# Optimization experiments

Measured on AMD Instinct MI355X. Metric: run time of the kernel, lower is better.

The kernel has to match this reference:

```python
import jax, jax.numpy as jnp
import numpy as np

ALPHA = 16.0
R = 8.0
SCALE = ALPHA / R  # scaling = alpha / r, same for every adapter


def setup_inputs() -> dict:
    key = jax.random.key(0)
    ks = jax.random.split(key, 5)
    B_, S, D = 4, 2048, 4096
    E, r = 8, 8
    x = jax.random.normal(ks[0], (B_, S, D), dtype=jnp.float32)
    W = jax.random.normal(ks[1], (D, D), dtype=jnp.float32) * (1.0 / np.sqrt(D))
    b = jax.random.normal(ks[2], (D,), dtype=jnp.float32) * 0.02
    A = jax.random.normal(ks[3], (E, r, D), dtype=jnp.float32) * (1.0 / np.sqrt(D))
    Bm = jax.random.normal(ks[4], (E, D, r), dtype=jnp.float32) * 0.02
    return {"x": x, "W": W, "b": b, "A": A, "B": Bm}


def reference(x, W, b, A, B):
    # base = F.linear(x, W, b)
    base = jnp.einsum('bsi,oi->bso', x, W) + b
    # lora_total = sum_e scale * (x @ A_e.T @ B_e.T); all experts stacked.
    # intermediate [B,S,E,r] is tiny (r=8)
    t = jnp.einsum('bsi,eri->bser', x, A)
    lora = jnp.einsum('bser,eor->bso', t, B) * SCALE
    return base + lora
```

## Files before the change

kernel.cpp:

```cpp
#include <hip/hip_runtime.h>
#include <hip/hip_bf16.h>

typedef unsigned short u16;
typedef __bf16 bf16x8 __attribute__((ext_vector_type(8)));
typedef float f32x4 __attribute__((ext_vector_type(4)));

constexpr int Mdim = 8192;
constexpr int Ndim = 4096;
constexpr int Kdim = 4096;
constexpr int ER   = 64;
constexpr float LSCALE = 2.0f;

__device__ __forceinline__ u16 f2bf(float f) {
    union { float f; unsigned u; } v; v.f = f;
    unsigned r = v.u + 0x7fffu + ((v.u >> 16) & 1u);
    return (u16)(r >> 16);
}

#define GLOAD_LDS16(g, l)                                             \
    __builtin_amdgcn_global_load_lds(                                 \
        (const __attribute__((address_space(1))) void*)(g),           \
        (__attribute__((address_space(3))) void*)(l), 16, 0, 0)

__global__ __launch_bounds__(256) void weff_kernel(
    const float* __restrict__ W, const float* __restrict__ A,
    const float* __restrict__ Bm, u16* __restrict__ Wb)
{
    __shared__ __align__(16) float sAc[ER][128];
    __shared__ __align__(16) float sBc[64][ER];

    const int t  = threadIdx.x;
    const int i0 = blockIdx.x * 128;
    const int o0 = blockIdx.y * 64;

#pragma unroll
    for (int p = 0; p < 8; ++p) {
        int lin = p * 1024 + t * 4;
        int er = lin >> 7, ci = lin & 127;
        *(float4*)&sAc[er][ci] = *(const float4*)(A + (size_t)er * Kdim + i0 + ci);
    }
    {
        int ol = t >> 2;
        int c  = (t & 3) * 16;
#pragma unroll
        for (int q = 0; q < 2; ++q) {
            int er = c + q * 8;
            int e  = er >> 3;
            const float* src = Bm + ((size_t)e * Ndim + (o0 + ol)) * 8;
            *(float4*)&sBc[ol][er]     = *(const float4*)(src);
            *(float4*)&sBc[ol][er + 4] = *(const float4*)(src + 4);
        }
    }
    __syncthreads();

    const int tx = t & 31;
    const int ty = t >> 5;
    float acc[8][4] = {};
#pragma unroll 4
    for (int er = 0; er < ER; ++er) {
        float4 a = *(const float4*)&sAc[er][tx * 4];
#pragma unroll
        for (int q = 0; q < 8; ++q) {
            float bv = sBc[q * 8 + ty][er];
            acc[q][0] += bv * a.x;
            acc[q][1] += bv * a.y;
            acc[q][2] += bv * a.z;
            acc[q][3] += bv * a.w;
        }
    }
#pragma unroll
    for (int q = 0; q < 8; ++q) {
        int o = o0 + q * 8 + ty;
        const float4 w = *(const float4*)(W + (size_t)o * Kdim + i0 + tx * 4);
        ushort4 st;
        st.x = f2bf(w.x + LSCALE * acc[q][0]);
        st.y = f2bf(w.y + LSCALE * acc[q][1]);
        st.z = f2bf(w.z + LSCALE * acc[q][2]);
        st.w = f2bf(w.w + LSCALE * acc[q][3]);
        *(ushort4*)(Wb + (size_t)o * Kdim + i0 + tx * 4) = st;
    }
}

__global__ __launch_bounds__(256) void cvt_x_kernel(
    const float* __restrict__ x, u16* __restrict__ xb)
{
    size_t i = (size_t)blockIdx.x * blockDim.x + threadIdx.x;
    const float4 v0 = *(const float4*)(x + i * 8);
    const float4 v1 = *(const float4*)(x + i * 8 + 4);
    uint4 o;
    o.x = (unsigned)f2bf(v0.x) | ((unsigned)f2bf(v0.y) << 16);
    o.y = (unsigned)f2bf(v0.z) | ((unsigned)f2bf(v0.w) << 16);
    o.z = (unsigned)f2bf(v1.x) | ((unsigned)f2bf(v1.y) << 16);
    o.w = (unsigned)f2bf(v1.z) | ((unsigned)f2bf(v1.w) << 16);
    *(uint4*)(xb + i * 8) = o;
}

constexpr int BM = 256, BN = 256, BK = 64;
constexpr int NT = Kdim / BK;

__global__ __launch_bounds__(512, 2) void gemm_bias_kernel(
    const u16* __restrict__ Xb, const u16* __restrict__ Wb,
    const float* __restrict__ bias, float* __restrict__ C)
{
    __shared__ __align__(16) u16 lds[65536];

    const int t    = threadIdx.x;
    const int lane = t & 63;
    const int wv   = t >> 6;
    const int wr   = wv >> 2;
    const int wc   = wv & 3;

    const int wg  = blockIdx.x;
    const int xcd = wg & 7, lid = wg >> 3;
    const int mt  = (xcd & 1) * 16 + (lid >> 2);
    const int ntl = (xcd >> 1) * 4 + (lid & 3);
    const int bm  = mt * BM;
    const int bn  = ntl * BN;

    u16* sA0 = lds;          u16* sA1 = lds + 16384;
    u16* sB0 = lds + 32768;  u16* sB1 = lds + 49152;

    const u16* aSrc[4]; const u16* bSrc[4]; int dOff[4];
#pragma unroll
    for (int i = 0; i < 4; ++i) {
        int c   = i * 512 + t;
        int cs  = c ^ (((c >> 5) & 1) << 1) ^ (((c >> 6) & 1) << 2);
        int row = c >> 3;
        int col = (cs & 7) * 8;
        aSrc[i] = Xb + (size_t)(bm + row) * Kdim + col;
        bSrc[i] = Wb + (size_t)(bn + row) * Kdim + col;
        dOff[i] = i * 4096 + t * 8;
    }

    const int rl  = (lane & 15) * 64;
    const int sx  = (((lane >> 2) & 1) << 4) | (((lane >> 3) & 1) << 5);
    const int cp0 = (((lane >> 4) * 8)) ^ sx;
    const int cp1 = (32 + (lane >> 4) * 8) ^ sx;
    const int aBase = wr * 8192 + rl;
    const int bBase = wc * 4096 + rl;

    f32x4 acc[8][4];
#pragma unroll
    for (int i = 0; i < 8; ++i)
#pragma unroll
        for (int j = 0; j < 4; ++j)
            acc[i][j] = f32x4{0.f, 0.f, 0.f, 0.f};

    bf16x8 af[4][2];
    bf16x8 bfr[4][2];

#define LOADA(SRC, MH)                                                        \
    _Pragma("unroll")                                                         \
    for (int mi = 0; mi < 4; ++mi) {                                          \
        af[mi][0] = *(const bf16x8*)&SRC[aBase + ((MH)*4 + mi) * 1024 + cp0]; \
        af[mi][1] = *(const bf16x8*)&SRC[aBase + ((MH)*4 + mi) * 1024 + cp1]; \
    }

#define LOADB(SRC, NH)                                                        \
    _Pragma("unroll")                                                         \
    for (int nl = 0; nl < 2; ++nl) {                                          \
        bfr[(NH)*2 + nl][0] = *(const bf16x8*)&SRC[bBase + ((NH)*2 + nl) * 1024 + cp0]; \
        bfr[(NH)*2 + nl][1] = *(const bf16x8*)&SRC[bBase + ((NH)*2 + nl) * 1024 + cp1]; \
    }

#define MQ(MH, NH)                                                            \
    __builtin_amdgcn_s_setprio(1);                                            \
    _Pragma("unroll")                                                         \
    for (int mi = 0; mi < 4; ++mi)                                            \
        _Pragma("unroll")                                                     \
        for (int nl = 0; nl < 2; ++nl) {                                      \
            acc[(MH)*4 + mi][(NH)*2 + nl] =                                   \
                __builtin_amdgcn_mfma_f32_16x16x32_bf16(                      \
                    af[mi][0], bfr[(NH)*2 + nl][0],                           \
                    acc[(MH)*4 + mi][(NH)*2 + nl], 0, 0, 0);                  \
            acc[(MH)*4 + mi][(NH)*2 + nl] =                                   \
                __builtin_amdgcn_mfma_f32_16x16x32_bf16(                      \
                    af[mi][1], bfr[(NH)*2 + nl][1],                           \
                    acc[(MH)*4 + mi][(NH)*2 + nl], 0, 0, 0);                  \
        }                                                                     \
    __builtin_amdgcn_s_setprio(0);

#define ITER(CURA, CURB, NXA, NXB, DOISS, VMS)                                \
    {                                                                         \
        if (DOISS) {                                                          \
            _Pragma("unroll")                                                 \
            for (int i = 0; i < 4; ++i)                                       \
                GLOAD_LDS16(aSrc[i] + koff, (NXA) + dOff[i]);                 \
            _Pragma("unroll")                                                 \
            for (int i = 0; i < 4; ++i)                                       \
                GLOAD_LDS16(bSrc[i] + koff, (NXB) + dOff[i]);                 \
            koff += 64;                                                       \
        }                                                                     \
        asm volatile("s_waitcnt vmcnt(" VMS ")" ::: "memory");                \
        __builtin_amdgcn_s_barrier();                                         \
        asm volatile("" ::: "memory");                                        \
        LOADA(CURA, 0); LOADB(CURB, 0); MQ(0, 0);                             \
        LOADB(CURB, 1); MQ(0, 1);                                             \
        LOADA(CURA, 1); MQ(1, 1);                                             \
        MQ(1, 0);                                                             \
        asm volatile("s_waitcnt lgkmcnt(0)" ::: "memory");                    \
        __builtin_amdgcn_s_barrier();                                         \
        asm volatile("" ::: "memory");                                        \
    }

#pragma unroll
    for (int i = 0; i < 4; ++i) GLOAD_LDS16(aSrc[i], sA0 + dOff[i]);
#pragma unroll
    for (int i = 0; i < 4; ++i) GLOAD_LDS16(bSrc[i], sB0 + dOff[i]);

    int koff = 64;

#pragma unroll 1
    for (int t2 = 0; t2 < NT - 2; t2 += 2) {
        ITER(sA0, sB0, sA1, sB1, 1, "8");
        ITER(sA1, sB1, sA0, sB0, 1, "8");
    }
    ITER(sA0, sB0, sA1, sB1, 1, "8");
    ITER(sA1, sB1, sA0, sB0, 0, "0");

#undef ITER
#undef MQ
#undef LOADB
#undef LOADA

#pragma unroll
    for (int ni = 0; ni < 4; ++ni) {
        const int col = bn + wc * 64 + ni * 16 + (lane & 15);
        const float bv = bias[col];
#pragma unroll
        for (int mi = 0; mi < 8; ++mi) {
            const int rbase = bm + wr * 128 + mi * 16 + (lane >> 4) * 4;
#pragma unroll
            for (int j = 0; j < 4; ++j)
                C[(size_t)(rbase + j) * Ndim + col] = acc[mi][ni][j] + bv;
        }
    }
}

__global__ __launch_bounds__(256) void naive_row_kernel(
    const float* __restrict__ x, const float* __restrict__ W,
    const float* __restrict__ bias, const float* __restrict__ A,
    const float* __restrict__ Bm, float* __restrict__ out)
{
    __shared__ float sx[Kdim];
    __shared__ float st[ER];
    const int m = blockIdx.x;
    const float* xr = x + (size_t)m * Kdim;
    for (int i = threadIdx.x; i < Kdim; i += 256) sx[i] = xr[i];
    __syncthreads();
    if (threadIdx.x < ER) {
        const float* ar = A + (size_t)threadIdx.x * Kdim;
        float s = 0.f;
        for (int i = 0; i < Kdim; ++i) s += sx[i] * ar[i];
        st[threadIdx.x] = s;
    }
    __syncthreads();
    for (int o = threadIdx.x; o < Ndim; o += 256) {
        const float* wr = W + (size_t)o * Kdim;
        float s = bias[o];
        for (int i = 0; i < Kdim; ++i) s += sx[i] * wr[i];
        float l = 0.f;
        for (int e = 0; e < 8; ++e) {
            const float* bp = Bm + ((size_t)e * Ndim + o) * 8;
            for (int r = 0; r < 8; ++r) l += st[e * 8 + r] * bp[r];
        }
        out[(size_t)m * Ndim + o] = s + LSCALE * l;
    }
}

extern "C" void kernel_launch(void* const* d_in, const int* in_sizes, int n_in,
                              void* d_out, int out_size, void* d_ws, size_t ws_size,
                              hipStream_t stream)
{
    const float* x  = (const float*)d_in[0];
    const float* W  = (const float*)d_in[1];
    const float* b  = (const float*)d_in[2];
    const float* A  = (const float*)d_in[3];
    const float* Bm = (const float*)d_in[4];
    float* out = (float*)d_out;

    const size_t xb_bytes = (size_t)Mdim * Kdim * 2;
    const size_t wb_bytes = (size_t)Ndim * Kdim * 2;

    if (ws_size >= xb_bytes + wb_bytes) {
        u16* Xb = (u16*)d_ws;
        u16* Wb = (u16*)((char*)d_ws + xb_bytes);
        cvt_x_kernel<<<(Mdim * (size_t)Kdim) / 8 / 256, 256, 0, stream>>>(x, Xb);
        weff_kernel<<<dim3(Kdim / 128, Ndim / 64), 256, 0, stream>>>(W, A, Bm, Wb);
        gemm_bias_kernel<<<dim3((Mdim / BM) * (Ndim / BN)), 512, 0, stream>>>(Xb, Wb, b, out);
    } else {
        naive_row_kernel<<<Mdim, 256, 0, stream>>>(x, W, b, A, Bm, out);
    }
}
```

Measured before the change: 327.3 us.

## Restructure GEMM main loop with barrier-fenced LDS reads and unified swizzled buffers

The main bf16 GEMM loop now keeps one combined A+B LDS buffer per stage and uses a simpler XOR swizzle for both the global-to-LDS copy and the fragment reads. Each iteration is split into phases: fragment loads, then explicit lgkmcnt waits and sched_barriers, each phase separated by workgroup barriers. This controls how LDS reads interleave with MFMA across waves and fixes the instruction order against compiler reordering. The cost is many more s_barrier calls per k-step, which can stall waves and reduce latency hiding.

```diff
diff --git a/kernel.cpp b/kernel.cpp
--- a/kernel.cpp
+++ b/kernel.cpp
@@ -117,27 +117,25 @@
     const int bm  = mt * BM;
     const int bn  = ntl * BN;
 
-    u16* sA0 = lds;          u16* sA1 = lds + 16384;
-    u16* sB0 = lds + 32768;  u16* sB1 = lds + 49152;
-
-    const u16* aSrc[4]; const u16* bSrc[4]; int dOff[4];
-#pragma unroll
-    for (int i = 0; i < 4; ++i) {
-        int c   = i * 512 + t;
-        int cs  = c ^ (((c >> 5) & 1) << 1) ^ (((c >> 6) & 1) << 2);
-        int row = c >> 3;
-        int col = (cs & 7) * 8;
-        aSrc[i] = Xb + (size_t)(bm + row) * Kdim + col;
-        bSrc[i] = Wb + (size_t)(bn + row) * Kdim + col;
-        dOff[i] = i * 4096 + t * 8;
-    }
-
-    const int rl  = (lane & 15) * 64;
-    const int sx  = (((lane >> 2) & 1) << 4) | (((lane >> 3) & 1) << 5);
-    const int cp0 = (((lane >> 4) * 8)) ^ sx;
-    const int cp1 = (32 + (lane >> 4) * 8) ^ sx;
-    const int aBase = wr * 8192 + rl;
-    const int bBase = wc * 4096 + rl;
+    u16* b0 = lds;
+    u16* b1 = lds + 32768;
+
+    const u16* gSrc[8]; int dOff[8];
+#pragma unroll
+    for (int i = 0; i < 8; ++i) {
+        const int sub = i & 3;
+        const int isB = i >> 2;
+        const int c   = sub * 512 + t;
+        const int row = c >> 3;
+        const int scl = ((c ^ row) & 7) * 8;
+        gSrc[i] = (isB ? Wb + (size_t)(bn + row) * Kdim
+                       : Xb + (size_t)(bm + row) * Kdim) + scl;
+        dOff[i] = isB * 16384 + c * 8;
+    }
+
+    const int fr  = lane & 15;
+    const int cp0 = (((lane >> 4)    ) ^ (lane & 7)) * 8;
+    const int cp1 = (((lane >> 4) + 4) ^ (lane & 7)) * 8;
 
     f32x4 acc[8][4];
 #pragma unroll
@@ -149,18 +147,21 @@
     bf16x8 af[4][2];
     bf16x8 bfr[4][2];
 
-#define LOADA(SRC, MH)                                                        \
+#define DS_AF(BUF, MH)                                                        \
     _Pragma("unroll")                                                         \
     for (int mi = 0; mi < 4; ++mi) {                                          \
-        af[mi][0] = *(const bf16x8*)&SRC[aBase + ((MH)*4 + mi) * 1024 + cp0]; \
-        af[mi][1] = *(const bf16x8*)&SRC[aBase + ((MH)*4 + mi) * 1024 + cp1]; \
-    }
-
-#define LOADB(SRC, NH)                                                        \
+        const int rb = (wr * 128 + (MH) * 64 + mi * 16 + fr) * 64;            \
+        af[mi][0] = *(const bf16x8*)&(BUF)[rb + cp0];                         \
+        af[mi][1] = *(const bf16x8*)&(BUF)[rb + cp1];                         \
+    }
+
+#define DS_BF(BUF, NH)                                                        \
     _Pragma("unroll")                                                         \
     for (int nl = 0; nl < 2; ++nl) {                                          \
-        bfr[(NH)*2 + nl][0] = *(const bf16x8*)&SRC[bBase + ((NH)*2 + nl) * 1024 + cp0]; \
-        bfr[(NH)*2 + nl][1] = *(const bf16x8*)&SRC[bBase + ((NH)*2 + nl) * 1024 + cp1]; \
+        const int ni = (NH) * 2 + nl;                                         \
+        const int rb = 16384 + (wc * 64 + ni * 16 + fr) * 64;                 \
+        bfr[ni][0] = *(const bf16x8*)&(BUF)[rb + cp0];                        \
+        bfr[ni][1] = *(const bf16x8*)&(BUF)[rb + cp1];                        \
     }
 
 #define MQ(MH, NH)                                                            \
@@ -169,59 +170,62 @@
     for (int mi = 0; mi < 4; ++mi)                                            \
         _Pragma("unroll")                                                     \
         for (int nl = 0; nl < 2; ++nl) {                                      \
-            acc[(MH)*4 + mi][(NH)*2 + nl] =                                   \
-                __builtin_amdgcn_mfma_f32_16x16x32_bf16(                      \
-                    af[mi][0], bfr[(NH)*2 + nl][0],                           \
-                    acc[(MH)*4 + mi][(NH)*2 + nl], 0, 0, 0);                  \
-            acc[(MH)*4 + mi][(NH)*2 + nl] =                                   \
-                __builtin_amdgcn_mfma_f32_16x16x32_bf16(                      \
-                    af[mi][1], bfr[(NH)*2 + nl][1],                           \
-                    acc[(MH)*4 + mi][(NH)*2 + nl], 0, 0, 0);                  \
+            const int ni = (NH) * 2 + nl;                                     \
+            acc[(MH)*4 + mi][ni] = __builtin_amdgcn_mfma_f32_16x16x32_bf16(   \
+                af[mi][0], bfr[ni][0], acc[(MH)*4 + mi][ni], 0, 0, 0);        \
+            acc[(MH)*4 + mi][ni] = __builtin_amdgcn_mfma_f32_16x16x32_bf16(   \
+                af[mi][1], bfr[ni][1], acc[(MH)*4 + mi][ni], 0, 0, 0);        \
         }                                                                     \
     __builtin_amdgcn_s_setprio(0);
 
-#define ITER(CURA, CURB, NXA, NXB, DOISS, VMS)                                \
+#define FENCE asm volatile("" ::: "memory")
+#define BAR   __builtin_amdgcn_s_barrier(); FENCE
+#define LGKM0 asm volatile("s_waitcnt lgkmcnt(0)" ::: "memory");              \
+              __builtin_amdgcn_sched_barrier(0)
+
+#define ITER(CUR, NXT, DOISS, VMS)                                            \
     {                                                                         \
         if (DOISS) {                                                          \
             _Pragma("unroll")                                                 \
-            for (int i = 0; i < 4; ++i)                                       \
-                GLOAD_LDS16(aSrc[i] + koff, (NXA) + dOff[i]);                 \
-            _Pragma("unroll")                                                 \
-            for (int i = 0; i < 4; ++i)                                       \
-                GLOAD_LDS16(bSrc[i] + koff, (NXB) + dOff[i]);                 \
+            for (int i = 0; i < 8; ++i)                                       \
+                GLOAD_LDS16(gSrc[i] + koff, (NXT) + dOff[i]);                 \
             koff += 64;                                                       \
         }                                                                     \
         asm volatile("s_waitcnt vmcnt(" VMS ")" ::: "memory");                \
-        __builtin_amdgcn_s_barrier();                                         \
-        asm volatile("" ::: "memory");                                        \
-        LOADA(CURA, 0); LOADB(CURB, 0); MQ(0, 0);                             \
-        LOADB(CURB, 1); MQ(0, 1);                                             \
-        LOADA(CURA, 1); MQ(1, 1);                                             \
+        BAR;                                                                  \
+        DS_AF(CUR, 0); DS_BF(CUR, 0);                                         \
+        asm volatile("s_waitcnt lgkmcnt(8)" ::: "memory");                    \
+        BAR;                                                                  \
+        LGKM0; MQ(0, 0);                                                      \
+        BAR;                                                                  \
+        DS_BF(CUR, 1);                                                        \
+        BAR;                                                                  \
+        LGKM0; MQ(0, 1);                                                      \
+        BAR;                                                                  \
+        DS_AF(CUR, 1);                                                        \
+        BAR;                                                                  \
+        LGKM0; MQ(1, 1);                                                      \
+        BAR;                                                                  \
         MQ(1, 0);                                                             \
-        asm volatile("s_waitcnt lgkmcnt(0)" ::: "memory");                    \
-        __builtin_amdgcn_s_barrier();                                         \
-        asm volatile("" ::: "memory");                                        \
-    }
-
-#pragma unroll
-    for (int i = 0; i < 4; ++i) GLOAD_LDS16(aSrc[i], sA0 + dOff[i]);
-#pragma unroll
-    for (int i = 0; i < 4; ++i) GLOAD_LDS16(bSrc[i], sB0 + dOff[i]);
+    }
+
+#pragma unroll
+    for (int i = 0; i < 8; ++i) GLOAD_LDS16(gSrc[i], b0 + dOff[i]);
 
     int koff = 64;
 
 #pragma unroll 1
-    for (int t2 = 0; t2 < NT - 2; t2 += 2) {
-        ITER(sA0, sB0, sA1, sB1, 1, "8");
-        ITER(sA1, sB1, sA0, sB0, 1, "8");
-    }
-    ITER(sA0, sB0, sA1, sB1, 1, "8");
-    ITER(sA1, sB1, sA0, sB0, 0, "0");
+    for (int t2 = 0; t2 < (NT - 2) / 2; ++t2) {
+        ITER(b0, b1, 1, "8");
+        ITER(b1, b0, 1, "8");
+    }
+    ITER(b0, b1, 1, "8");
+    ITER(b1, b0, 0, "0");
 
 #undef ITER
 #undef MQ
-#undef LOADB
-#undef LOADA
+#undef DS_BF
+#undef DS_AF
 
 #pragma unroll
     for (int ni = 0; ni < 4; ++ni) {
```

Result: faster. 312.1 us (-4.6%).
